# Kernel optimization log

Hardware: AMD Instinct MI355X
Metric: run time of the kernel (lower is better)

## Reference

```python
import jax, jax.numpy as jnp
import numpy as np

N_NODES = 100000
N_EDGES = 3200000
IN_F = 128
HID = 32


def setup_inputs() -> dict:
    key = jax.random.key(0)
    k = jax.random.split(key, 8)
    x = jax.random.normal(k[0], (N_NODES, IN_F), dtype=jnp.float32)
    edge_index = jax.random.randint(k[1], (2, N_EDGES), 0, N_NODES, dtype=jnp.int64)
    edge_weight = jax.random.uniform(k[2], (N_EDGES,), dtype=jnp.float32)
    # GCN conv weight (in -> 32) and bias, then Linear(32 -> 1)
    s1 = 1.0 / np.sqrt(IN_F)
    s2 = 1.0 / np.sqrt(HID)
    W1 = jax.random.uniform(k[3], (IN_F, HID), dtype=jnp.float32, minval=-s1, maxval=s1)
    b1 = jax.random.uniform(k[4], (HID,), dtype=jnp.float32, minval=-s1, maxval=s1)
    W2 = jax.random.uniform(k[5], (HID, 1), dtype=jnp.float32, minval=-s2, maxval=s2)
    b2 = jax.random.uniform(k[6], (1,), dtype=jnp.float32, minval=-s2, maxval=s2)
    return {"x": x, "edge_index": edge_index, "edge_weight": edge_weight,
            "W1": W1, "b1": b1, "W2": W2, "b2": b2}


def gcn_conv(x, edge_index, edge_weight, W, b):
    N = x.shape[0]
    src = edge_index[0]
    dst = edge_index[1]
    loop = jnp.arange(N, dtype=edge_index.dtype)
    row = jnp.concatenate([dst, loop])  # aggregation targets
    col = jnp.concatenate([src, loop])  # message sources
    w = jnp.concatenate([edge_weight, jnp.ones((N,), dtype=x.dtype)])
    deg = jax.ops.segment_sum(w, row, num_segments=N)
    dinv = jnp.where(deg > 0, deg ** -0.5, 0.0).astype(x.dtype)
    norm = dinv[row] * w * dinv[col]  # [E+N]
    h = x @ W  # [N, 32]  transform before gather (cheaper)
    msgs = norm[:, None] * h[col]  # [E+N, 32]
    agg = jax.ops.segment_sum(msgs, row, num_segments=N)  # [N, 32]
    return agg + b


def reference(x, edge_index, edge_weight, W1, b1, W2, b2):
    h = gcn_conv(x, edge_index, edge_weight, W1, b1)
    h = jax.nn.relu(h)
    return h @ W2 + b2  # [N, 1]
```

## Files before the change

### kernel.cpp

```cpp
#include <hip/hip_runtime.h>
#include <hip/hip_bf16.h>
#include <hip/hip_fp16.h>

#define NN 100000
#define NE 3200000
#define IN_F 128
#define HID 32

#define NB 782
#define NBP1 (NB + 1)
#define BNODES 128
#define PBLK 782
#define EPB 4096
#define SSPAN 5120

typedef __hip_bfloat16 bf16;
typedef __attribute__((ext_vector_type(8))) short s16x8;
typedef __attribute__((ext_vector_type(4))) float f32x4;

__global__ __launch_bounds__(512) void k_part(const int* __restrict__ ei,
                                              const float* __restrict__ ew,
                                              int* __restrict__ offs,
                                              unsigned* __restrict__ raw1,
                                              unsigned short* __restrict__ raw2) {
    __shared__ int hist[NB];
    __shared__ int start[NB];
    __shared__ int wtot[8];
    __shared__ unsigned sp1[EPB];
    __shared__ unsigned short sp2[EPB];

    int t = threadIdx.x;
    int blk = blockIdx.x;
    for (int b = t; b < NB; b += 512) hist[b] = 0;
    __syncthreads();

    unsigned pk[8]; unsigned short hw[8]; int bkt[8];
    int base_e = blk * EPB;
#pragma unroll
    for (int j = 0; j < 8; j++) {
        int e = base_e + j * 512 + t;
        if (e < NE) {
            int src = __builtin_nontemporal_load(ei + e);
            int dst = __builtin_nontemporal_load(ei + NE + e);
            float w = __builtin_nontemporal_load(ew + e);
            bkt[j] = dst >> 7;
            pk[j] = (unsigned)src | ((unsigned)(dst & 127) << 20);
            hw[j] = __half_as_ushort(__float2half(w));
        } else bkt[j] = -1;
    }
#pragma unroll
    for (int j = 0; j < 8; j++)
        if (bkt[j] >= 0) atomicAdd(&hist[bkt[j]], 1);
    __syncthreads();

    int e0 = 2 * t, e1 = 2 * t + 1;
    int h0 = (e0 < NB) ? hist[e0] : 0;
    int h1 = (e1 < NB) ? hist[e1] : 0;
    int psum = h0 + h1;
    int lane = t & 63;
    int incl = psum;
#pragma unroll
    for (int off = 1; off < 64; off <<= 1) {
        int up = __shfl_up(incl, off, 64);
        if (lane >= off) incl += up;
    }
    int wid = t >> 6;
    if (lane == 63) wtot[wid] = incl;
    __syncthreads();
    int woff = 0;
    for (int wj = 0; wj < wid; wj++) woff += wtot[wj];
    int exc = woff + incl - psum;
    if (e0 < NB) start[e0] = exc;
    if (e1 < NB) start[e1] = exc + h0;
    __syncthreads();

    int total = start[NB - 1] + hist[NB - 1];

    int* orow = offs + (size_t)blk * NBP1;
    for (int b = t; b < NB; b += 512) orow[b] = start[b];
    if (t == 0) orow[NB] = total;
    __syncthreads();

#pragma unroll
    for (int j = 0; j < 8; j++) {
        if (bkt[j] >= 0) {
            int pos = atomicAdd(&start[bkt[j]], 1);
            sp1[pos] = pk[j];
            sp2[pos] = hw[j];
        }
    }
    __syncthreads();

    unsigned* r1 = raw1 + (size_t)blk * EPB;
    unsigned short* r2 = raw2 + (size_t)blk * EPB;
    for (int i = t; i < total; i += 512) {
        r1[i] = sp1[i];
        r2[i] = sp2[i];
    }
}

__global__ __launch_bounds__(256) void k_sort(const int* __restrict__ offs,
                                              const unsigned* __restrict__ raw1,
                                              const unsigned short* __restrict__ raw2,
                                              unsigned* __restrict__ srt1,
                                              unsigned short* __restrict__ srt2,
                                              int* __restrict__ rowstart,
                                              int* __restrict__ rowcnt,
                                              float* __restrict__ dinv) {
    __shared__ unsigned se1[SSPAN];
    __shared__ unsigned short se2[SSPAN];
    __shared__ int hist[BNODES];
    __shared__ float wsum[BNODES];
    __shared__ int scanbuf[BNODES];
    __shared__ int cur[BNODES];
    __shared__ int gcur;

    int t = threadIdx.x;
    int b = blockIdx.x;
    if (t < BNODES) { hist[t] = 0; wsum[t] = 1.0f; }
    if (t == 0) gcur = 0;
    __syncthreads();

    for (int blk = t; blk < PBLK; blk += 256) {
        const int* orow = offs + (size_t)blk * NBP1;
        int o0 = orow[b], o1 = orow[b + 1];
        int n = o1 - o0;
        if (n > 0) {
            int base = atomicAdd(&gcur, n);
            const unsigned* r1 = raw1 + (size_t)blk * EPB + o0;
            const unsigned short* r2 = raw2 + (size_t)blk * EPB + o0;
            for (int i = 0; i < n; i++) {
                int pos = base + i;
                if (pos < SSPAN) {
                    unsigned p = r1[i];
                    unsigned short w = r2[i];
                    se1[pos] = p; se2[pos] = w;
                    int dl = (p >> 20) & 127;
                    atomicAdd(&hist[dl], 1);
                    atomicAdd(&wsum[dl], __half2float(__ushort_as_half(w)));
                }
            }
        }
    }
    __syncthreads();
    int total = min(gcur, SSPAN);

    if (t < BNODES) scanbuf[t] = hist[t];
    __syncthreads();
    for (int off = 1; off < BNODES; off <<= 1) {
        int v = 0;
        if (t < BNODES && t >= off) v = scanbuf[t - off];
        __syncthreads();
        if (t < BNODES) scanbuf[t] += v;
        __syncthreads();
    }

    int obase = b * SSPAN;
    if (t < BNODES) {
        int binstart = scanbuf[t] - hist[t];
        cur[t] = binstart;
        int node = b * BNODES + t;
        if (node < NN) {
            rowstart[node] = obase + binstart;
            rowcnt[node]   = hist[t];
            dinv[node]     = rsqrtf(wsum[t]);
        }
    }
    __syncthreads();

    for (int i = t; i < total; i += 256) {
        unsigned p = se1[i];
        int dl = (p >> 20) & 127;
        int pos = atomicAdd(&cur[dl], 1);
        srt1[obase + pos] = p & 0xFFFFF;
        srt2[obase + pos] = se2[i];
    }
}

__global__ void k_w1frag(const float* __restrict__ W1, unsigned short* __restrict__ wfrag) {
    int lane = threadIdx.x;
    int q = lane >> 4;
    int n0 = lane & 15;
#pragma unroll
    for (int ks = 0; ks < 4; ks++) {
#pragma unroll
        for (int nt = 0; nt < 2; nt++) {
            int fi = ks * 2 + nt;
            int n = n0 + 16 * nt;
#pragma unroll
            for (int j = 0; j < 8; j++) {
                int k = ks * 32 + q * 8 + j;
                float v = W1[k * HID + n];
                __hip_bfloat16 bv = __float2bfloat16(v);
                wfrag[((size_t)fi * 64 + lane) * 8 + j] = *(unsigned short*)&bv;
            }
        }
    }
}

__global__ __launch_bounds__(256) void k_hs(const float* __restrict__ x,
                                            const unsigned short* __restrict__ wfrag,
                                            const float* __restrict__ dinv,
                                            bf16* __restrict__ hs) {
    int t = threadIdx.x;
    int lane = t & 63;
    int wv = t >> 6;
    int base = blockIdx.x * 64 + wv * 16;
    int m = lane & 15;
    int q = lane >> 4;
    int node = base + m;

    s16x8 wf[8];
    const s16x8* wp = (const s16x8*)wfrag;
#pragma unroll
    for (int fi = 0; fi < 8; fi++) wf[fi] = wp[fi * 64 + lane];

    f32x4 acc0 = {0.f, 0.f, 0.f, 0.f};
    f32x4 acc1 = {0.f, 0.f, 0.f, 0.f};

    const float* rowp = x + (size_t)node * IN_F + q * 8;
    bool valid = (node < NN);

#pragma unroll
    for (int ks = 0; ks < 4; ks++) {
        float4 f0 = {0,0,0,0}, f1 = {0,0,0,0};
        if (valid) {
            const float4* xr = (const float4*)(rowp + ks * 32);
            f0 = xr[0]; f1 = xr[1];
        }
        union { s16x8 v; unsigned u32[4]; } af;
        __hip_bfloat162 p0 = __float22bfloat162_rn({f0.x, f0.y});
        __hip_bfloat162 p1 = __float22bfloat162_rn({f0.z, f0.w});
        __hip_bfloat162 p2 = __float22bfloat162_rn({f1.x, f1.y});
        __hip_bfloat162 p3 = __float22bfloat162_rn({f1.z, f1.w});
        af.u32[0] = *(unsigned*)&p0;
        af.u32[1] = *(unsigned*)&p1;
        af.u32[2] = *(unsigned*)&p2;
        af.u32[3] = *(unsigned*)&p3;
        acc0 = __builtin_amdgcn_mfma_f32_16x16x32_bf16(af.v, wf[ks * 2 + 0], acc0, 0, 0, 0);
        acc1 = __builtin_amdgcn_mfma_f32_16x16x32_bf16(af.v, wf[ks * 2 + 1], acc1, 0, 0, 0);
    }

    int f = lane & 15;
#pragma unroll
    for (int r = 0; r < 4; r++) {
        int n2 = base + q * 4 + r;
        if (n2 < NN) {
            float dv = dinv[n2];
            hs[(size_t)n2 * HID + f]      = __float2bfloat16(dv * acc0[r]);
            hs[(size_t)n2 * HID + f + 16] = __float2bfloat16(dv * acc1[r]);
        }
    }
}

__global__ __launch_bounds__(256) void k_agg(const int* __restrict__ rowstart,
                                             const int* __restrict__ rowcnt,
                                             const unsigned* __restrict__ srcs,
                                             const unsigned short* __restrict__ wts,
                                             const bf16* __restrict__ hs,
                                             const float* __restrict__ dinv,
                                             const float* __restrict__ b1, const float* __restrict__ W2,
                                             const float* __restrict__ b2, float* __restrict__ out) {
    int t = threadIdx.x;
    int l = t & 15;
    int node = blockIdx.x * 16 + (t >> 4);
    int rs = rowstart[node];
    int re = rs + rowcnt[node];
    const __hip_bfloat162* hs2 = (const __hip_bfloat162*)hs;
    float acc0 = 0.f, acc1 = 0.f;

    for (int base = rs; base < re; base += 16) {
        int idx = base + l;
        int sreg = 0; float wreg = 0.f;
        if (idx < re) {
            sreg = (int)srcs[idx];
            wreg = __half2float(__ushort_as_half(wts[idx]));
        }
        int m = min(16, re - base);
        int j = 0;
        for (; j + 8 <= m; j += 8) {
            int s0 = __shfl(sreg, j + 0, 16), s1 = __shfl(sreg, j + 1, 16);
            int s2 = __shfl(sreg, j + 2, 16), s3 = __shfl(sreg, j + 3, 16);
            int s4 = __shfl(sreg, j + 4, 16), s5 = __shfl(sreg, j + 5, 16);
            int s6 = __shfl(sreg, j + 6, 16), s7 = __shfl(sreg, j + 7, 16);
            float w0 = __shfl(wreg, j + 0, 16), w1 = __shfl(wreg, j + 1, 16);
            float w2 = __shfl(wreg, j + 2, 16), w3 = __shfl(wreg, j + 3, 16);
            float w4 = __shfl(wreg, j + 4, 16), w5 = __shfl(wreg, j + 5, 16);
            float w6 = __shfl(wreg, j + 6, 16), w7 = __shfl(wreg, j + 7, 16);
            __hip_bfloat162 h0 = hs2[(size_t)s0 * 16 + l];
            __hip_bfloat162 h1 = hs2[(size_t)s1 * 16 + l];
            __hip_bfloat162 h2 = hs2[(size_t)s2 * 16 + l];
            __hip_bfloat162 h3 = hs2[(size_t)s3 * 16 + l];
            __hip_bfloat162 h4 = hs2[(size_t)s4 * 16 + l];
            __hip_bfloat162 h5 = hs2[(size_t)s5 * 16 + l];
            __hip_bfloat162 h6 = hs2[(size_t)s6 * 16 + l];
            __hip_bfloat162 h7 = hs2[(size_t)s7 * 16 + l];
            float2 f0 = __bfloat1622float2(h0); acc0 += w0 * f0.x; acc1 += w0 * f0.y;
            float2 f1 = __bfloat1622float2(h1); acc0 += w1 * f1.x; acc1 += w1 * f1.y;
            float2 f2 = __bfloat1622float2(h2); acc0 += w2 * f2.x; acc1 += w2 * f2.y;
            float2 f3 = __bfloat1622float2(h3); acc0 += w3 * f3.x; acc1 += w3 * f3.y;
            float2 f4 = __bfloat1622float2(h4); acc0 += w4 * f4.x; acc1 += w4 * f4.y;
            float2 f5 = __bfloat1622float2(h5); acc0 += w5 * f5.x; acc1 += w5 * f5.y;
            float2 f6 = __bfloat1622float2(h6); acc0 += w6 * f6.x; acc1 += w6 * f6.y;
            float2 f7 = __bfloat1622float2(h7); acc0 += w7 * f7.x; acc1 += w7 * f7.y;
        }
        for (; j < m; j++) {
            int s = __shfl(sreg, j, 16);
            float w = __shfl(wreg, j, 16);
            float2 fv = __bfloat1622float2(hs2[(size_t)s * 16 + l]);
            acc0 += w * fv.x; acc1 += w * fv.y;
        }
    }

    float2 fs = __bfloat1622float2(hs2[(size_t)node * 16 + l]);
    float dv = dinv[node];
    float v0 = dv * (acc0 + fs.x) + b1[2 * l];
    float v1 = dv * (acc1 + fs.y) + b1[2 * l + 1];
    v0 = fmaxf(v0, 0.f);
    v1 = fmaxf(v1, 0.f);
    float psum = v0 * W2[2 * l] + v1 * W2[2 * l + 1];
#pragma unroll
    for (int m2 = 8; m2 >= 1; m2 >>= 1) psum += __shfl_xor(psum, m2, 16);
    if (l == 0) out[node] = psum + b2[0];
}

extern "C" void kernel_launch(void* const* d_in, const int* in_sizes, int n_in,
                              void* d_out, int out_size, void* d_ws, size_t ws_size,
                              hipStream_t stream) {
    const float* x  = (const float*)d_in[0];
    const int*   ei = (const int*)d_in[1];
    const float* ew = (const float*)d_in[2];
    const float* W1 = (const float*)d_in[3];
    const float* b1 = (const float*)d_in[4];
    const float* W2 = (const float*)d_in[5];
    const float* b2 = (const float*)d_in[6];
    float* out = (float*)d_out;

    char* ws = (char*)d_ws;
    unsigned*       raw1     = (unsigned*)      (ws + 0);
    unsigned short* raw2     = (unsigned short*)(ws + 12812288);
    int*            offs     = (int*)           (ws + 19218432);
    unsigned*       srt1     = (unsigned*)      (ws + 21667840);
    unsigned short* srt2     = (unsigned short*)(ws + 37683200);
    int*            rowstart = (int*)           (ws + 45690880);
    int*            rowcnt   = (int*)           (ws + 46090880);
    float*          dinv     = (float*)         (ws + 46490880);
    bf16*           hs       = (bf16*)          (ws + 46890880);
    unsigned short* wfrag    = (unsigned short*)(ws + 53290880);

    k_w1frag<<<1, 64, 0, stream>>>(W1, wfrag);
    k_part<<<PBLK, 512, 0, stream>>>(ei, ew, offs, raw1, raw2);
    k_sort<<<NB, 256, 0, stream>>>(offs, raw1, raw2, srt1, srt2, rowstart, rowcnt, dinv);
    k_hs<<<(NN + 63) / 64, 256, 0, stream>>>(x, wfrag, dinv, hs);
    k_agg<<<NN / 16, 256, 0, stream>>>(rowstart, rowcnt, srt1, srt2, hs, dinv, b1, W2, b2, out);
}
```

Measured before the change: 248.2 us.

## Restructure edge bucketing: two-pass partition, transposed offsets, parallel gather in sort

The partition kernel now reads edges twice: a first pass builds the bucket histogram, a second pass re-reads them and scatters packed uint2 records (src|local dst, fp32 weight) straight to global memory, skipping the shared-memory staging. Blocks now cover 8192 edges each, halving the number of partition blocks. A new transpose kernel lays the per-block offsets out bucket-major, so the sort kernel can read its row of run lengths coalesced, prefix-scan them, and gather records with one thread per edge instead of a serial loop per run. The trade-off is extra edge-index reads, scattered global writes, one more kernel launch, fp32 weights in the intermediate buffer, and a smaller SSPAN cap on edges per bucket.

```diff
diff --git a/kernel.cpp b/kernel.cpp
--- a/kernel.cpp
+++ b/kernel.cpp
@@ -10,9 +10,9 @@
 #define NB 782
 #define NBP1 (NB + 1)
 #define BNODES 128
-#define PBLK 782
-#define EPB 4096
-#define SSPAN 5120
+#define PBLK 392
+#define EPB 8192
+#define SSPAN 4608
 
 typedef __hip_bfloat16 bf16;
 typedef __attribute__((ext_vector_type(8))) short s16x8;
@@ -21,36 +21,25 @@
 __global__ __launch_bounds__(512) void k_part(const int* __restrict__ ei,
                                               const float* __restrict__ ew,
                                               int* __restrict__ offs,
-                                              unsigned* __restrict__ raw1,
-                                              unsigned short* __restrict__ raw2) {
+                                              uint2* __restrict__ raw) {
     __shared__ int hist[NB];
     __shared__ int start[NB];
-    __shared__ int wtot[8];
-    __shared__ unsigned sp1[EPB];
-    __shared__ unsigned short sp2[EPB];
+    __shared__ int wtot8[8];
 
     int t = threadIdx.x;
     int blk = blockIdx.x;
     for (int b = t; b < NB; b += 512) hist[b] = 0;
     __syncthreads();
 
-    unsigned pk[8]; unsigned short hw[8]; int bkt[8];
     int base_e = blk * EPB;
 #pragma unroll
-    for (int j = 0; j < 8; j++) {
+    for (int j = 0; j < 16; j++) {
         int e = base_e + j * 512 + t;
         if (e < NE) {
-            int src = __builtin_nontemporal_load(ei + e);
             int dst = __builtin_nontemporal_load(ei + NE + e);
-            float w = __builtin_nontemporal_load(ew + e);
-            bkt[j] = dst >> 7;
-            pk[j] = (unsigned)src | ((unsigned)(dst & 127) << 20);
-            hw[j] = __half_as_ushort(__float2half(w));
-        } else bkt[j] = -1;
-    }
-#pragma unroll
-    for (int j = 0; j < 8; j++)
-        if (bkt[j] >= 0) atomicAdd(&hist[bkt[j]], 1);
+            atomicAdd(&hist[dst >> 7], 1);
+        }
+    }
     __syncthreads();
 
     int e0 = 2 * t, e1 = 2 * t + 1;
@@ -65,85 +54,120 @@
         if (lane >= off) incl += up;
     }
     int wid = t >> 6;
-    if (lane == 63) wtot[wid] = incl;
+    if (lane == 63) wtot8[wid] = incl;
     __syncthreads();
     int woff = 0;
-    for (int wj = 0; wj < wid; wj++) woff += wtot[wj];
+    for (int wj = 0; wj < wid; wj++) woff += wtot8[wj];
     int exc = woff + incl - psum;
     if (e0 < NB) start[e0] = exc;
     if (e1 < NB) start[e1] = exc + h0;
     __syncthreads();
 
     int total = start[NB - 1] + hist[NB - 1];
-
     int* orow = offs + (size_t)blk * NBP1;
     for (int b = t; b < NB; b += 512) orow[b] = start[b];
     if (t == 0) orow[NB] = total;
     __syncthreads();
 
 #pragma unroll
-    for (int j = 0; j < 8; j++) {
-        if (bkt[j] >= 0) {
-            int pos = atomicAdd(&start[bkt[j]], 1);
-            sp1[pos] = pk[j];
-            sp2[pos] = hw[j];
-        }
-    }
-    __syncthreads();
-
-    unsigned* r1 = raw1 + (size_t)blk * EPB;
-    unsigned short* r2 = raw2 + (size_t)blk * EPB;
-    for (int i = t; i < total; i += 512) {
-        r1[i] = sp1[i];
-        r2[i] = sp2[i];
-    }
-}
-
-__global__ __launch_bounds__(256) void k_sort(const int* __restrict__ offs,
-                                              const unsigned* __restrict__ raw1,
-                                              const unsigned short* __restrict__ raw2,
+    for (int j = 0; j < 16; j++) {
+        int e = base_e + j * 512 + t;
+        if (e < NE) {
+            int src = __builtin_nontemporal_load(ei + e);
+            int dst = __builtin_nontemporal_load(ei + NE + e);
+            float w = __builtin_nontemporal_load(ew + e);
+            int bkt = dst >> 7;
+            unsigned pk = (unsigned)src | ((unsigned)(dst & 127) << 20);
+            int pos = atomicAdd(&start[bkt], 1);
+            raw[(size_t)blk * EPB + pos] = make_uint2(pk, __float_as_uint(w));
+        }
+    }
+}
+
+__global__ __launch_bounds__(256) void k_trans(const int* __restrict__ in, int* __restrict__ out) {
+    __shared__ int tile[32][33];
+    int c0 = blockIdx.x * 32, r0 = blockIdx.y * 32;
+    int tx = threadIdx.x & 31, ty = threadIdx.x >> 5;
+    for (int i = ty; i < 32; i += 8) {
+        int r = r0 + i, c = c0 + tx;
+        if (r < PBLK && c < NBP1) tile[i][tx] = in[(size_t)r * NBP1 + c];
+    }
+    __syncthreads();
+    for (int i = ty; i < 32; i += 8) {
+        int c = c0 + i, r = r0 + tx;
+        if (c < NBP1 && r < PBLK) out[(size_t)c * PBLK + r] = tile[tx][i];
+    }
+}
+
+__global__ __launch_bounds__(256) void k_sort(const int* __restrict__ offsT,
+                                              const uint2* __restrict__ raw,
                                               unsigned* __restrict__ srt1,
                                               unsigned short* __restrict__ srt2,
                                               int* __restrict__ rowstart,
                                               int* __restrict__ rowcnt,
                                               float* __restrict__ dinv) {
-    __shared__ unsigned se1[SSPAN];
-    __shared__ unsigned short se2[SSPAN];
+    __shared__ uint2 se[SSPAN];
+    __shared__ unsigned short runid[SSPAN];
+    __shared__ int P[PBLK + 1];
+    __shared__ int O0[PBLK];
     __shared__ int hist[BNODES];
     __shared__ float wsum[BNODES];
     __shared__ int scanbuf[BNODES];
     __shared__ int cur[BNODES];
-    __shared__ int gcur;
+    __shared__ int wt4[4];
 
     int t = threadIdx.x;
     int b = blockIdx.x;
     if (t < BNODES) { hist[t] = 0; wsum[t] = 1.0f; }
-    if (t == 0) gcur = 0;
-    __syncthreads();
-
-    for (int blk = t; blk < PBLK; blk += 256) {
-        const int* orow = offs + (size_t)blk * NBP1;
-        int o0 = orow[b], o1 = orow[b + 1];
-        int n = o1 - o0;
-        if (n > 0) {
-            int base = atomicAdd(&gcur, n);
-            const unsigned* r1 = raw1 + (size_t)blk * EPB + o0;
-            const unsigned short* r2 = raw2 + (size_t)blk * EPB + o0;
-            for (int i = 0; i < n; i++) {
-                int pos = base + i;
-                if (pos < SSPAN) {
-                    unsigned p = r1[i];
-                    unsigned short w = r2[i];
-                    se1[pos] = p; se2[pos] = w;
-                    int dl = (p >> 20) & 127;
-                    atomicAdd(&hist[dl], 1);
-                    atomicAdd(&wsum[dl], __half2float(__ushort_as_half(w)));
-                }
-            }
-        }
-    }
-    __syncthreads();
-    int total = min(gcur, SSPAN);
+
+    int e0 = 2 * t, e1 = 2 * t + 1;
+    int l0 = 0, l1 = 0;
+    if (e0 < PBLK) {
+        int o0 = offsT[(size_t)b * PBLK + e0];
+        l0 = offsT[(size_t)(b + 1) * PBLK + e0] - o0;
+        O0[e0] = o0;
+    }
+    if (e1 < PBLK) {
+        int o1 = offsT[(size_t)b * PBLK + e1];
+        l1 = offsT[(size_t)(b + 1) * PBLK + e1] - o1;
+        O0[e1] = o1;
+    }
+    int psum = l0 + l1;
+    int lane = t & 63;
+    int incl = psum;
+#pragma unroll
+    for (int off = 1; off < 64; off <<= 1) {
+        int up = __shfl_up(incl, off, 64);
+        if (lane >= off) incl += up;
+    }
+    int wid = t >> 6;
+    if (lane == 63) wt4[wid] = incl;
+    __syncthreads();
+    int woff = 0;
+    for (int wj = 0; wj < wid; wj++) woff += wt4[wj];
+    int exc = woff + incl - psum;
+    if (e0 < PBLK) P[e0] = exc;
+    if (e1 < PBLK) P[e1] = exc + l0;
+    if (t == 0) P[PBLK] = wt4[0] + wt4[1] + wt4[2] + wt4[3];
+    __syncthreads();
+
+    int total = min(P[PBLK], SSPAN);
+
+    for (int r = t; r < PBLK; r += 256) {
+        int p0 = P[r], p1 = min(P[r + 1], SSPAN);
+        for (int i = p0; i < p1; i++) runid[i] = (unsigned short)r;
+    }
+    __syncthreads();
+
+    for (int d = t; d < total; d += 256) {
+        int r = runid[d];
+        uint2 rec = raw[(size_t)r * EPB + O0[r] + (d - P[r])];
+        se[d] = rec;
+        int dl = (rec.x >> 20) & 127;
+        atomicAdd(&hist[dl], 1);
+        atomicAdd(&wsum[dl], __uint_as_float(rec.y));
+    }
+    __syncthreads();
 
     if (t < BNODES) scanbuf[t] = hist[t];
     __syncthreads();
@@ -169,11 +193,11 @@
     __syncthreads();
 
     for (int i = t; i < total; i += 256) {
-        unsigned p = se1[i];
-        int dl = (p >> 20) & 127;
+        uint2 rec = se[i];
+        int dl = (rec.x >> 20) & 127;
         int pos = atomicAdd(&cur[dl], 1);
-        srt1[obase + pos] = p & 0xFFFFF;
-        srt2[obase + pos] = se2[i];
+        srt1[obase + pos] = rec.x & 0xFFFFF;
+        srt2[obase + pos] = __half_as_ushort(__float2half(__uint_as_float(rec.y)));
     }
 }
 
@@ -337,20 +361,21 @@
     float* out = (float*)d_out;
 
     char* ws = (char*)d_ws;
-    unsigned*       raw1     = (unsigned*)      (ws + 0);
-    unsigned short* raw2     = (unsigned short*)(ws + 12812288);
-    int*            offs     = (int*)           (ws + 19218432);
-    unsigned*       srt1     = (unsigned*)      (ws + 21667840);
-    unsigned short* srt2     = (unsigned short*)(ws + 37683200);
-    int*            rowstart = (int*)           (ws + 45690880);
-    int*            rowcnt   = (int*)           (ws + 46090880);
-    float*          dinv     = (float*)         (ws + 46490880);
-    bf16*           hs       = (bf16*)          (ws + 46890880);
-    unsigned short* wfrag    = (unsigned short*)(ws + 53290880);
+    uint2*          raw      = (uint2*)         (ws + 0);
+    int*            offs     = (int*)           (ws + 25690112);
+    int*            offsT    = (int*)           (ws + 26917888);
+    unsigned*       srt1     = (unsigned*)      (ws + 28145664);
+    unsigned short* srt2     = (unsigned short*)(ws + 42559488);
+    int*            rowstart = (int*)           (ws + 49766400);
+    int*            rowcnt   = (int*)           (ws + 50166400);
+    float*          dinv     = (float*)         (ws + 50566400);
+    bf16*           hs       = (bf16*)          (ws + 50966400);
+    unsigned short* wfrag    = (unsigned short*)(ws + 57366400);
 
     k_w1frag<<<1, 64, 0, stream>>>(W1, wfrag);
-    k_part<<<PBLK, 512, 0, stream>>>(ei, ew, offs, raw1, raw2);
-    k_sort<<<NB, 256, 0, stream>>>(offs, raw1, raw2, srt1, srt2, rowstart, rowcnt, dinv);
+    k_part<<<PBLK, 512, 0, stream>>>(ei, ew, offs, raw);
+    k_trans<<<dim3((NBP1 + 31) / 32, (PBLK + 31) / 32), 256, 0, stream>>>(offs, offsT);
+    k_sort<<<NB, 256, 0, stream>>>(offsT, raw, srt1, srt2, rowstart, rowcnt, dinv);
     k_hs<<<(NN + 63) / 64, 256, 0, stream>>>(x, wfrag, dinv, hs);
     k_agg<<<NN / 16, 256, 0, stream>>>(rowstart, rowcnt, srt1, srt2, hs, dinv, b1, W2, b2, out);
 }
```

After: 291.7 us. 17.5% more time.
